# Optimization experiments

Measured on AMD Instinct MI355X. Metric: run time of the kernel, lower is better.

## Reference

```python
import jax, jax.numpy as jnp
import numpy as np

K = 3           # kernel_size
P = 9           # patch_size (number of displacements per axis)
PAD = 1         # padding (keeps output spatial size == input)
DIL = 1         # dilation (kernel)
DILP = 1        # dilation_patch (displacement spacing)


def setup_inputs() -> dict:
    key = jax.random.key(0)
    noise = jax.random.normal(key, (8, 16, 192, 192), dtype=jnp.float32)
    return {"noise": noise}


def _correlation(noise):
    # SpatialCorrelationSampler(noise, noise) semantics:
    # out[b, di, dj, y, x] = sum_{c, ki, kj}
    #     n1[b,c, y-PAD+ki*DIL,          x-PAD+kj*DIL] *
    #     n2[b,c, y-PAD+ki*DIL+ddy,      x-PAD+kj*DIL+ddx]
    # with ddy = (di - P//2)*DILP, zero padding outside bounds.
    # Equivalent: per-displacement channel-summed product, then K x K box sum.
    B, C, H, W = noise.shape
    r = (P // 2) * DILP  # max displacement radius
    pad2 = jnp.pad(noise, ((0, 0), (0, 0), (r, r), (r, r)))
    prods = []
    for di in range(P):
        for dj in range(P):
            oy, ox = di * DILP, dj * DILP
            shifted = pad2[:, :, oy:oy + H, ox:ox + W]  # zero beyond borders
            prods.append(jnp.sum(noise * shifted, axis=1))  # [B,H,W]
    corr = jnp.stack(prods, axis=1)  # [B, P*P, H, W]
    # K x K box sum with zero padding (= kernel window accumulation)
    ones = jnp.ones((1, 1, K, K), corr.dtype)
    corr = jax.lax.conv_general_dilated(
        corr.reshape(B * P * P, 1, H, W), ones,
        window_strides=(1, 1), padding=((PAD, PAD), (PAD, PAD)),
        rhs_dilation=(DIL, DIL),
        dimension_numbers=("NCHW", "OIHW", "NCHW"))
    # module normalizes by ch and kernel_size**2, then views to [B, P*P, H, W]
    return corr.reshape(B, P * P, H, W) / (C * K * K)


def reference(noise):
    return _correlation(noise)
```

## Files before the change

### kernel.cpp

```cpp
#include <hip/hip_runtime.h>

#define HH 192
#define WW 192
#define CC 16
#define HW (HH * WW)
#define TH 30
#define TW 24
#define RS 44
#define PCHUNKS 512
#define PLANEF (PCHUNKS*4)
#define RSS 28
#define SMEMF 8192

__device__ float g_zero16[4] = {0.f, 0.f, 0.f, 0.f};

__device__ __forceinline__ void gload16(const void* g, void* l) {
    __builtin_amdgcn_global_load_lds(
        (const __attribute__((address_space(1))) void*)g,
        (__attribute__((address_space(3))) void*)l, 16, 0, 0);
}

__global__ __launch_bounds__(256, 3)
void noise_corr_kernel(const float* __restrict__ noise, float* __restrict__ out) {
    __shared__ float smem[SMEMF];
    float* const planes = smem;
    float* const rsum   = smem;

    const int tid = threadIdx.x;
    const int r   = tid >> 3;
    const int g   = tid & 7;
    const int bx  = blockIdx.x % 9;
    const int by  = blockIdx.x / 9;
    const int grp = blockIdx.y;
    const int b   = blockIdx.z;

    const int oymin = grp ? -1 : -4;
    const int NOY   = grp ? 2 : 3;
    const int rmin  = oymin - 1;
    const int NR    = TH + 2 - oymin;
    const int nitems = NR * 11;

    const int y0 = -4 + by * TH;
    const int x0 = -4 + bx * TW;
    const int yy = r - 1;
    const int xs = (g << 2) - 4;

    const float* nb = noise + (size_t)b * CC * HW;
    const char* zp = (const char*)g_zero16;

    int goff[2]; bool gok[2];
    #pragma unroll
    for (int k = 0; k < 2; ++k) {
        const int i  = tid + (k << 8);
        const int rr = i / 11;
        const int q  = i - rr * 11;
        const int gy = y0 + rmin + rr;
        const int gx = x0 - 8 + (q << 2);
        gok[k]  = (i < nitems) && ((unsigned)gy < HH) && ((unsigned)gx <= (WW - 4));
        goff[k] = (gy * WW + gx) * 4;
    }

    float acc[3][9][4];
    #pragma unroll
    for (int t = 0; t < 3; ++t)
        #pragma unroll
        for (int o = 0; o < 9; ++o) {
            acc[t][o][0] = 0.f; acc[t][o][1] = 0.f;
            acc[t][o][2] = 0.f; acc[t][o][3] = 0.f;
        }

    #pragma unroll
    for (int p = 0; p < 3; ++p) {
        const char* base = (const char*)(nb + (size_t)p * HW);
        char* lb = (char*)planes + p * (PLANEF * 4);
        gload16(gok[0] ? base + goff[0] : zp, lb + (tid << 4));
        gload16(gok[1] ? base + goff[1] : zp, lb + ((tid + 256) << 4));
    }

    const int ci = yy - rmin;

    for (int c = 0; c < CC; ++c) {
        if (c == CC - 1) {
            asm volatile("s_waitcnt vmcnt(0)" ::: "memory");
        } else if (c == CC - 2) {
            asm volatile("s_waitcnt vmcnt(2)" ::: "memory");
        } else {
            asm volatile("s_waitcnt vmcnt(4)" ::: "memory");
        }
        __builtin_amdgcn_sched_barrier(0);
        __builtin_amdgcn_s_barrier();
        if (c + 3 < CC) {
            const char* base = (const char*)(nb + (size_t)(c + 3) * HW);
            char* lb = (char*)planes + ((c + 3) & 3) * (PLANEF * 4);
            gload16(gok[0] ? base + goff[0] : zp, lb + (tid << 4));
            gload16(gok[1] ? base + goff[1] : zp, lb + ((tid + 256) << 4));
        }
        const float* pl = planes + (c & 3) * PLANEF;
        const float4 cen4 = *(const float4*)&pl[ci * RS + xs + 8];
        const float cen[4] = {cen4.x, cen4.y, cen4.z, cen4.w};
        #pragma unroll
        for (int t = 0; t < 3; ++t) {
            if (t < NOY) {
                const float* sr = &pl[(ci + oymin + t) * RS + xs + 4];
                float sh[12];
                *(float4*)&sh[0] = *(const float4*)&sr[0];
                *(float4*)&sh[4] = *(const float4*)&sr[4];
                *(float4*)&sh[8] = *(const float4*)&sr[8];
                #pragma unroll
                for (int o = 0; o < 9; ++o)
                    #pragma unroll
                    for (int j = 0; j < 4; ++j)
                        acc[t][o][j] += cen[j] * sh[o + j];
            }
        }
    }

    const float inv = 1.0f / 144.0f;
    float* outb = out + (size_t)b * 81 * HW;
    const int yb  = tid / 6;
    const int xgb = tid % 6;

    #pragma unroll
    for (int t = 0; t < 3; ++t) {
        if (t < NOY) {
            const int oy = oymin + t;
            __syncthreads();
            #pragma unroll
            for (int o = 0; o < 9; ++o) {
                const float a0 = acc[t][o][0], a1 = acc[t][o][1];
                const float a2 = acc[t][o][2], a3 = acc[t][o][3];
                const float left  = __shfl_up(a3, 1);
                const float right = __shfl_down(a0, 1);
                if (g >= 1 && g <= 6) {
                    float4 v;
                    v.x = left + a0 + a1;
                    v.y = a0 + a1 + a2;
                    v.z = a1 + a2 + a3;
                    v.w = a2 + a3 + right;
                    *(float4*)&rsum[(o * 32 + r) * RSS + ((g - 1) << 2)] = v;
                }
            }
            __syncthreads();
            if (tid < 180) {
                const int gy = y0 + yb;
                const int gx = x0 + (xgb << 2);
                const bool dok = ((unsigned)gy < HH) && ((unsigned)gx <= (WW - 4));
                const int my = gy + oy;
                #pragma unroll
                for (int o = 0; o < 9; ++o) {
                    const float* rp = &rsum[(o * 32 + yb) * RSS + (xgb << 2)];
                    const float4 s0 = *(const float4*)&rp[0];
                    const float4 s1 = *(const float4*)&rp[RSS];
                    const float4 s2 = *(const float4*)&rp[2 * RSS];
                    float4 s;
                    s.x = (s0.x + s1.x + s2.x) * inv;
                    s.y = (s0.y + s1.y + s2.y) * inv;
                    s.z = (s0.z + s1.z + s2.z) * inv;
                    s.w = (s0.w + s1.w + s2.w) * inv;
                    if (dok)
                        *(float4*)&outb[((size_t)((oy + 4) * 9 + o)) * HW + gy * WW + gx] = s;
                    if (oy < 0 && (unsigned)my < HH) {
                        float* mp = &outb[((size_t)((4 - oy) * 9 + (8 - o))) * HW + (size_t)my * WW];
                        const float sv[4] = {s.x, s.y, s.z, s.w};
                        const int mx0 = gx + (o - 4);
                        #pragma unroll
                        for (int j = 0; j < 4; ++j) {
                            const int mx = mx0 + j;
                            if ((unsigned)mx < WW) mp[mx] = sv[j];
                        }
                    }
                }
            }
        }
    }
}

extern "C" void kernel_launch(void* const* d_in, const int* in_sizes, int n_in,
                              void* d_out, int out_size, void* d_ws, size_t ws_size,
                              hipStream_t stream) {
    const float* noise = (const float*)d_in[0];
    float* out = (float*)d_out;
    dim3 grid(9 * 7, 2, 8);
    noise_corr_kernel<<<grid, 256, 0, stream>>>(noise, out);
}
```

Before: 163.9 us.

## Give each wavefront a private LDS staging ring to drop block barriers

Measured after the change: 161.7 us. Within noise of the previous version (-1.4%).

```diff
diff --git a/kernel.cpp b/kernel.cpp
--- a/kernel.cpp
+++ b/kernel.cpp
@@ -6,11 +6,11 @@
 #define HW (HH * WW)
 #define TH 30
 #define TW 24
-#define RS 44
-#define PCHUNKS 512
-#define PLANEF (PCHUNKS*4)
+#define RSW 44
+#define SLOTB 3072
+#define WSTRB (3 * SLOTB)
 #define RSS 28
-#define SMEMF 8192
+#define SMEMF 9216
 
 __device__ float g_zero16[4] = {0.f, 0.f, 0.f, 0.f};
 
@@ -23,40 +23,44 @@
 __global__ __launch_bounds__(256, 3)
 void noise_corr_kernel(const float* __restrict__ noise, float* __restrict__ out) {
     __shared__ float smem[SMEMF];
-    float* const planes = smem;
-    float* const rsum   = smem;
+    float* const rsum = smem;
 
-    const int tid = threadIdx.x;
-    const int r   = tid >> 3;
-    const int g   = tid & 7;
-    const int bx  = blockIdx.x % 9;
-    const int by  = blockIdx.x / 9;
-    const int grp = blockIdx.y;
-    const int b   = blockIdx.z;
+    const int tid  = threadIdx.x;
+    const int w    = tid >> 6;
+    const int lane = tid & 63;
+    const int r    = tid >> 3;
+    const int g    = tid & 7;
+    const int lr   = lane >> 3;
+    const int bx   = blockIdx.x % 9;
+    const int by   = blockIdx.x / 9;
+    const int grp  = blockIdx.y;
+    const int b    = blockIdx.z;
 
     const int oymin = grp ? -1 : -4;
     const int NOY   = grp ? 2 : 3;
     const int rmin  = oymin - 1;
-    const int NR    = TH + 2 - oymin;
-    const int nitems = NR * 11;
+    const int NRW   = grp ? 9 : 12;
+    const int KL    = grp ? 2 : 3;
 
     const int y0 = -4 + by * TH;
     const int x0 = -4 + bx * TW;
-    const int yy = r - 1;
     const int xs = (g << 2) - 4;
 
     const float* nb = noise + (size_t)b * CC * HW;
-    const char* zp = (const char*)g_zero16;
+    const char* zp  = (const char*)g_zero16;
+    char* const wb  = (char*)smem + w * WSTRB;
 
-    int goff[2]; bool gok[2];
+    const int wrow0 = y0 + rmin + (w << 3);
+
+    int goff[3]; bool gok[3];
     #pragma unroll
-    for (int k = 0; k < 2; ++k) {
-        const int i  = tid + (k << 8);
+    for (int k = 0; k < 3; ++k) {
+        const int i  = (k << 6) + lane;
         const int rr = i / 11;
         const int q  = i - rr * 11;
-        const int gy = y0 + rmin + rr;
+        const int gy = wrow0 + rr;
         const int gx = x0 - 8 + (q << 2);
-        gok[k]  = (i < nitems) && ((unsigned)gy < HH) && ((unsigned)gx <= (WW - 4));
+        gok[k]  = (i < NRW * 11) && ((unsigned)gy < HH) && ((unsigned)gx <= (WW - 4));
         goff[k] = (gy * WW + gx) * 4;
     }
 
@@ -70,38 +74,45 @@
         }
 
     #pragma unroll
-    for (int p = 0; p < 3; ++p) {
+    for (int p = 0; p < 2; ++p) {
         const char* base = (const char*)(nb + (size_t)p * HW);
-        char* lb = (char*)planes + p * (PLANEF * 4);
-        gload16(gok[0] ? base + goff[0] : zp, lb + (tid << 4));
-        gload16(gok[1] ? base + goff[1] : zp, lb + ((tid + 256) << 4));
+        char* lb = wb + p * SLOTB;
+        #pragma unroll
+        for (int k = 0; k < 3; ++k)
+            if (k < KL)
+                gload16(gok[k] ? base + goff[k] : zp, lb + (((k << 6) + lane) << 4));
     }
 
-    const int ci = yy - rmin;
+    const int ci_l = lr - 1 - rmin;
 
+    int scur = 0, spre = 2;
     for (int c = 0; c < CC; ++c) {
-        if (c == CC - 1) {
+        if (c + 2 < CC) {
+            const char* base = (const char*)(nb + (size_t)(c + 2) * HW);
+            char* lb = wb + spre * SLOTB;
+            #pragma unroll
+            for (int k = 0; k < 3; ++k)
+                if (k < KL)
+                    gload16(gok[k] ? base + goff[k] : zp, lb + (((k << 6) + lane) << 4));
+        }
+        if (c < CC - 2) {
+            if (grp) asm volatile("s_waitcnt vmcnt(4)" ::: "memory");
+            else     asm volatile("s_waitcnt vmcnt(6)" ::: "memory");
+        } else if (c == CC - 2) {
+            if (grp) asm volatile("s_waitcnt vmcnt(2)" ::: "memory");
+            else     asm volatile("s_waitcnt vmcnt(3)" ::: "memory");
+        } else {
             asm volatile("s_waitcnt vmcnt(0)" ::: "memory");
-        } else if (c == CC - 2) {
-            asm volatile("s_waitcnt vmcnt(2)" ::: "memory");
-        } else {
-            asm volatile("s_waitcnt vmcnt(4)" ::: "memory");
         }
         __builtin_amdgcn_sched_barrier(0);
-        __builtin_amdgcn_s_barrier();
-        if (c + 3 < CC) {
-            const char* base = (const char*)(nb + (size_t)(c + 3) * HW);
-            char* lb = (char*)planes + ((c + 3) & 3) * (PLANEF * 4);
-            gload16(gok[0] ? base + goff[0] : zp, lb + (tid << 4));
-            gload16(gok[1] ? base + goff[1] : zp, lb + ((tid + 256) << 4));
-        }
-        const float* pl = planes + (c & 3) * PLANEF;
-        const float4 cen4 = *(const float4*)&pl[ci * RS + xs + 8];
+
+        const float* pl = (const float*)(wb + scur * SLOTB);
+        const float4 cen4 = *(const float4*)&pl[ci_l * RSW + xs + 8];
         const float cen[4] = {cen4.x, cen4.y, cen4.z, cen4.w};
         #pragma unroll
         for (int t = 0; t < 3; ++t) {
             if (t < NOY) {
-                const float* sr = &pl[(ci + oymin + t) * RS + xs + 4];
+                const float* sr = &pl[(ci_l + oymin + t) * RSW + xs + 4];
                 float sh[12];
                 *(float4*)&sh[0] = *(const float4*)&sr[0];
                 *(float4*)&sh[4] = *(const float4*)&sr[4];
@@ -113,6 +124,8 @@
                         acc[t][o][j] += cen[j] * sh[o + j];
             }
         }
+        scur = (scur == 2) ? 0 : scur + 1;
+        spre = (spre == 2) ? 0 : spre + 1;
     }
 
     const float inv = 1.0f / 144.0f;
```
